# Optimization experiments

Measured on AMD Instinct MI355X. Metric: run time of the kernel, lower is better.

The kernel has to match this reference:

```python
import jax, jax.numpy as jnp
import numpy as np

TAU = 0.96      # init_tau
N_OUT = 48      # readout neurons (last n_out of the merged population)
V_TH = 1.0      # LIF firing threshold

@jax.custom_vjp
def spike_fn(v):
    # Heaviside firing with triangle surrogate gradient
    return (v >= V_TH).astype(v.dtype)

def _spike_fwd(v):
    return spike_fn(v), v

def _spike_bwd(v, g):
    # TriangleCall surrogate: grad = max(0, 1 - |v - v_th|)
    return (g * jnp.maximum(0.0, 1.0 - jnp.abs(v - V_TH)),)

spike_fn.defvjp(_spike_fwd, _spike_bwd)


def setup_inputs() -> dict:
    key = jax.random.key(0)
    k1, k2, k3, k4 = jax.random.split(key, 4)
    B, T, n_in = 256, 100, 512
    n_hidden, n_out = 2000, 48
    N = n_hidden + n_out  # 2048
    x = jax.random.uniform(k1, (B, T, n_in), dtype=jnp.float32)
    # nn.Linear default init U(-1/sqrt(fan_in), 1/sqrt(fan_in)), scaled by 3, frozen
    bound = 1.0 / np.sqrt(n_in)
    W_fc = 3.0 * jax.random.uniform(k2, (N, n_in), minval=-bound, maxval=bound, dtype=jnp.float32)
    recurrent = jax.random.uniform(k3, (N, N), dtype=jnp.float32) / np.sqrt(N)
    mask = jnp.ones((N, N), jnp.float32) - jnp.eye(N, dtype=jnp.float32)  # no self-connections
    binary = (jax.random.uniform(k4, (N, N)) > 0.3).astype(jnp.float32)
    return {"x": x, "W_fc": W_fc, "recurrent": recurrent, "mask": mask, "binary": binary}


def reference(x, W_fc, recurrent, mask, binary):
    B = x.shape[0]
    N = recurrent.shape[0]
    eff_rec = recurrent * mask * binary                    # [N, N]
    # feed-forward currents for all timesteps at once: [B, T, N]
    cur_in = jnp.einsum('btn,mn->btm', x, W_fc)

    def step(carry, c_t):
        mem, spike = carry                                 # each [B, N]
        cur = c_t + spike @ eff_rec                        # recurrent drive
        mem = TAU * mem * (1.0 - spike) + cur              # LIF decay + hard reset
        spike = spike_fn(mem)
        return (mem, spike), spike[:, -N_OUT:]

    init = (jnp.zeros((B, N), x.dtype), jnp.zeros((B, N), x.dtype))
    _, outs = jax.lax.scan(step, init, jnp.swapaxes(cur_in, 0, 1))  # [T, B, n_out]
    return jnp.swapaxes(outs, 0, 1)                        # [B, T, n_out]
```

## Files before the change

### kernel.cpp

```cpp
#include <hip/hip_runtime.h>

typedef unsigned short u16;
typedef signed char s8;
typedef __attribute__((ext_vector_type(8))) short short8;
typedef __attribute__((ext_vector_type(4))) float f32x4;
typedef __attribute__((ext_vector_type(4))) unsigned short u16x4;
typedef __attribute__((ext_vector_type(4))) int i32x4;
typedef __attribute__((ext_vector_type(4))) unsigned int u32x4;

#define TT 100
#define NB 256
#define NN 2048
#define KREC 4096
#define NPRE 2
#define EPS 0.25f
#define WMAXC 0.1325826f
#define INV_SW (127.0f / WMAXC)
#define S_DEQ (WMAXC / 16129.0f)

#define OFF_WH    0ull
#define OFF_WL    2097152ull
#define OFF_WQ    4194304ull
#define OFF_XH4   5242880ull
#define OFF_XL4   6291456ull
#define OFF_XQ    7340032ull
#define OFF_BC    20447232ull
#define OFF_COLS  37224448ull
#define OFF_PARTC 37232640ull
#define OFF_FFPRE 37494784ull
#define OFF_SPK   45883392ull
#define OFF_MEMB  46931968ull
#define OFF_PART  49029120ull
#define OFF_FLAGS 65806336ull
#define OFF_AF    65806400ull
#define OFF_SYNC  65806912ull

__device__ __forceinline__ u16 f2bf(float f){
    unsigned int x = __float_as_uint(f);
    x += 0x7fffu + ((x >> 16) & 1u);
    return (u16)(x >> 16);
}
__device__ __forceinline__ float bf2f(u16 u){
    return __uint_as_float(((unsigned int)u) << 16);
}

__global__ void prep_all(const float* __restrict__ x, const float* __restrict__ Wfc,
                         const float* __restrict__ rec, const float* __restrict__ msk,
                         const float* __restrict__ bin,
                         u16* __restrict__ Wh, u16* __restrict__ Wl, s8* __restrict__ Wq,
                         u16* __restrict__ xh4, u16* __restrict__ xl4, s8* __restrict__ xq,
                         u16* __restrict__ Bc, float* __restrict__ partc)
{
    __shared__ u16 hs[64][66];
    __shared__ u16 ls[64][66];
    __shared__ float redc[4][64];
    int bid = blockIdx.x;
    if (bid < 6400){
        int idx = bid * 256 + threadIdx.x;
        int b = idx / (TT * 64);
        int r = idx - b * (TT * 64);
        int t = r >> 6;
        int c = r & 63;
        const float* gx = x + ((size_t)b * TT + t) * 512 + (c << 3);
        f32x4 f0 = *reinterpret_cast<const f32x4*>(gx);
        f32x4 f1 = *reinterpret_cast<const f32x4*>(gx + 4);
        unsigned long long q = 0;
        #pragma unroll
        for (int i = 0; i < 4; ++i)
            q |= (unsigned long long)(unsigned)__float2int_rn(f0[i] * 127.0f) << (8 * i);
        #pragma unroll
        for (int i = 0; i < 4; ++i)
            q |= (unsigned long long)(unsigned)__float2int_rn(f1[i] * 127.0f) << (8 * (i + 4));
        size_t o = ((size_t)t * NB + b) * 512 + (c << 3);
        *reinterpret_cast<unsigned long long*>(xq + o) = q;
        if (t < 4){
            short8 vh, vl;
            #pragma unroll
            for (int i = 0; i < 4; ++i){
                u16 h0 = f2bf(f0[i]);
                vh[i] = (short)h0; vl[i] = (short)f2bf(f0[i] - bf2f(h0));
                u16 h1 = f2bf(f1[i]);
                vh[i + 4] = (short)h1; vl[i + 4] = (short)f2bf(f1[i] - bf2f(h1));
            }
            *reinterpret_cast<short8*>(xh4 + o) = vh;
            *reinterpret_cast<short8*>(xl4 + o) = vl;
        }
    } else if (bid < 10496){
        int idx = (bid - 6400) * 256 + threadIdx.x;
        float v = Wfc[idx];
        u16 h = f2bf(v);
        Wh[idx] = h;
        Wl[idx] = f2bf(v - bf2f(h));
        Wq[idx] = (s8)__float2int_rn(v * INV_SW);
    } else {
        int r2 = bid - 10496;
        int bx = r2 & 31, by = r2 >> 5;
        int tid = threadIdx.x;
        int tm = tid & 63, t4 = tid >> 6;
        int m0 = bx * 64, n0 = by * 64;
        float accl = 0.f;
        #pragma unroll
        for (int j = 0; j < 16; ++j){
            int nl = t4 + j * 4;
            size_t gi = (size_t)(n0 + nl) * NN + m0 + tm;
            float e = rec[gi] * msk[gi] * bin[gi];
            u16 h = f2bf(e);
            hs[nl][tm] = h;
            ls[nl][tm] = f2bf(e - bf2f(h));
            accl += e;
        }
        redc[t4][tm] = accl;
        __syncthreads();
        if (t4 == 0)
            partc[(size_t)by * NN + m0 + tm] =
                redc[0][tm] + redc[1][tm] + redc[2][tm] + redc[3][tm];
        #pragma unroll
        for (int j = 0; j < 16; ++j){
            int ml = t4 + j * 4;
            size_t o = (size_t)(m0 + ml) * KREC + n0 + tm;
            Bc[o]        = hs[tm][ml];
            Bc[o + 2048] = ls[tm][ml];
        }
    }
}

__global__ __launch_bounds__(512, 2) void fused_gemm(const s8* __restrict__ xq,
    const s8* __restrict__ Wq, const u16* __restrict__ xh4, const u16* __restrict__ xl4,
    const u16* __restrict__ Wh, const u16* __restrict__ Wl,
    const float* __restrict__ partc, float* __restrict__ cs, float* __restrict__ ffpre,
    int* __restrict__ AF, float* __restrict__ out)
{
    __shared__ u16 Ab[2][4096];
    __shared__ u16 Bb[2][8192];
    __shared__ float csL[256];
    __shared__ int redH[8];
    const int tid = threadIdx.x, lane = tid & 63, w = tid >> 6;
    const int l7 = lane & 7, l8 = lane >> 3;
    const int bid = blockIdx.x;

    if (bid >= 192){
        const int bid2 = bid - 192;
        const int logical = (bid2 & 7) * 200 + (bid2 >> 3);
        const int mt = logical >> 3;
        const int bn = logical & 7;
        const int wm = w >> 2, wn = w & 3;

        if (tid < 256){
            float s = 0.f;
            #pragma unroll
            for (int c = 0; c < 32; ++c) s += partc[(size_t)c * NN + bn * 256 + tid];
            csL[tid] = s;
        }

        char* As_ = reinterpret_cast<char*>(Ab);
        char* Bs_ = reinterpret_cast<char*>(Bb);
        const int row_s = tid >> 2, gr = tid & 3;
        const int swA = ((row_s << 6) | (gr << 4)) ^ ((row_s & 7) << 4);
        const s8* gA = xq + (size_t)(mt * 128 + row_s) * 512 + gr * 16;
        int swB[2];
        const s8* gBp[2];
        #pragma unroll
        for (int j = 0; j < 2; ++j){
            int rb = j * 128 + row_s;
            swB[j] = ((rb << 6) | (gr << 4)) ^ ((rb & 7) << 4);
            gBp[j] = Wq + (size_t)(bn * 256 + rb) * 512 + gr * 16;
        }

        *reinterpret_cast<u32x4*>(As_ + swA) = *reinterpret_cast<const u32x4*>(gA);
        #pragma unroll
        for (int j = 0; j < 2; ++j)
            *reinterpret_cast<u32x4*>(Bs_ + swB[j]) = *reinterpret_cast<const u32x4*>(gBp[j]);
        u32x4 na  = *reinterpret_cast<const u32x4*>(gA + 64);
        u32x4 nb0 = *reinterpret_cast<const u32x4*>(gBp[0] + 64);
        u32x4 nb1 = *reinterpret_cast<const u32x4*>(gBp[1] + 64);
        __syncthreads();

        i32x4 acc[4][4];
        #pragma unroll
        for (int mi = 0; mi < 4; ++mi)
            #pragma unroll
            for (int ni = 0; ni < 4; ++ni) acc[mi][ni] = (i32x4){0, 0, 0, 0};

        const int kgb = (lane >> 4) << 4;
        #pragma unroll
        for (int kt = 0; kt < 8; ++kt){
            const int sel = kt & 1;
            if (kt < 7){
                const int os = sel ^ 1;
                *reinterpret_cast<u32x4*>(As_ + os * 8192 + swA) = na;
                *reinterpret_cast<u32x4*>(Bs_ + os * 16384 + swB[0]) = nb0;
                *reinterpret_cast<u32x4*>(Bs_ + os * 16384 + swB[1]) = nb1;
                if (kt + 2 < 8){
                    na  = *reinterpret_cast<const u32x4*>(gA + (kt + 2) * 64);
                    nb0 = *reinterpret_cast<const u32x4*>(gBp[0] + (kt + 2) * 64);
                    nb1 = *reinterpret_cast<const u32x4*>(gBp[1] + (kt + 2) * 64);
                }
            }
            const char* ab = As_ + sel * 8192;
            const char* bb3 = Bs_ + sel * 16384;
            i32x4 afr[4];
            #pragma unroll
            for (int mi = 0; mi < 4; ++mi){
                int r = wm * 64 + mi * 16 + (lane & 15);
                int off = ((r << 6) | kgb) ^ ((r & 7) << 4);
                afr[mi] = *reinterpret_cast<const i32x4*>(ab + off);
            }
            #pragma unroll
            for (int ni = 0; ni < 4; ++ni){
                int r = wn * 64 + ni * 16 + (lane & 15);
                int off = ((r << 6) | kgb) ^ ((r & 7) << 4);
                i32x4 bfr = *reinterpret_cast<const i32x4*>(bb3 + off);
                #pragma unroll
                for (int mi = 0; mi < 4; ++mi)
                    acc[mi][ni] = __builtin_amdgcn_mfma_i32_16x16x64_i8(afr[mi], bfr, acc[mi][ni], 0, 0, 0);
            }
            __syncthreads();
        }

        const int r4 = (lane >> 4) << 2;
        const int cfrag = lane & 15;
        const int t_out = mt >> 1;
        int ok = 1;
        #pragma unroll
        for (int mi = 0; mi < 4; ++mi)
            #pragma unroll
            for (int ni = 0; ni < 4; ++ni){
                int nl = wn * 64 + ni * 16 + cfrag;
                int n = bn * 256 + nl;
                float csv = csL[nl];
                #pragma unroll
                for (int jj = 0; jj < 4; ++jj){
                    int m = mt * 128 + wm * 64 + mi * 16 + r4 + jj;
                    float v = (float)acc[mi][ni][jj] * S_DEQ + csv;
                    ok &= (v >= 1.0f + EPS) ? 1 : 0;
                    if (bn == 7 && n >= 2000){
                        int b = m & 255;
                        out[((size_t)b * TT + t_out) * 48 + (n - 2000)] = (v >= 1.0f) ? 1.f : 0.f;
                    }
                }
            }
        unsigned long long bb = __ballot(ok != 0);
        if (lane == 0) redH[w] = (bb == ~0ull) ? 1 : 0;
        __syncthreads();
        if (tid == 0){
            int a = 1;
            #pragma unroll
            for (int i = 0; i < 8; ++i) a &= redH[i];
            atomicAnd(&AF[t_out], a ? ~0 : 0);
        }
    } else {
        const int bn = bid & 15;
        const int mt = bid >> 4;
        const int wm = w >> 2, wn = w & 3;

        if (mt == 0 && tid < 128){
            float s = 0.f;
            #pragma unroll
            for (int c = 0; c < 32; ++c) s += partc[(size_t)c * NN + bn * 128 + tid];
            cs[bn * 128 + tid] = s;
        }

        auto load_tile = [&](int kt, short8* pa, short8* pb){
            int reg = kt >> 3;
            int kk = (kt & 7) * 64;
            const u16* ab = (reg == 2) ? xl4 : xh4;
            const u16* bb2 = (reg == 1) ? Wl : Wh;
            {
                int row = w * 8 + l8;
                pa[0] = *reinterpret_cast<const short8*>(ab + (size_t)(mt * 64 + row) * 512 + kk + (l7 << 3));
            }
            #pragma unroll
            for (int j = 0; j < 2; ++j){
                int chunk = w * 2 + j;
                int row = chunk * 8 + l8;
                pb[j] = *reinterpret_cast<const short8*>(bb2 + (size_t)(bn * 128 + row) * 512 + kk + (l7 << 3));
            }
        };
        auto write_tile = [&](int sel, const short8* pa, const short8* pb){
            *reinterpret_cast<short8*>(&Ab[sel][w * 512 + l8 * 64 + ((l7 ^ l8) << 3)]) = pa[0];
            #pragma unroll
            for (int j = 0; j < 2; ++j){
                int chunk = w * 2 + j;
                *reinterpret_cast<short8*>(&Bb[sel][chunk * 512 + l8 * 64 + ((l7 ^ l8) << 3)]) = pb[j];
            }
        };

        f32x4 zero = {0.f, 0.f, 0.f, 0.f};
        f32x4 acc[2][2];
        #pragma unroll
        for (int mi = 0; mi < 2; ++mi)
            #pragma unroll
            for (int ni = 0; ni < 2; ++ni) acc[mi][ni] = zero;

        short8 ra[1], rb[2], na[1], nb[2];
        load_tile(0, ra, rb);
        write_tile(0, ra, rb);
        __syncthreads();

        for (int kt = 0; kt < 24; ++kt){
            int sel = kt & 1;
            if (kt + 1 < 24) load_tile(kt + 1, na, nb);
            #pragma unroll
            for (int kk2 = 0; kk2 < 2; ++kk2){
                int ke = kk2 * 32 + ((lane >> 4) << 3);
                short8 af[2], bfr[2];
                #pragma unroll
                for (int mi = 0; mi < 2; ++mi){
                    int row = wm * 32 + mi * 16 + (lane & 15);
                    int byte = (row * 128 + ke * 2) ^ ((row & 7) << 4);
                    af[mi] = *reinterpret_cast<const short8*>(reinterpret_cast<const char*>(Ab[sel]) + byte);
                }
                #pragma unroll
                for (int ni = 0; ni < 2; ++ni){
                    int row = wn * 32 + ni * 16 + (lane & 15);
                    int byte = (row * 128 + ke * 2) ^ ((row & 7) << 4);
                    bfr[ni] = *reinterpret_cast<const short8*>(reinterpret_cast<const char*>(Bb[sel]) + byte);
                }
                #pragma unroll
                for (int mi = 0; mi < 2; ++mi)
                    #pragma unroll
                    for (int ni = 0; ni < 2; ++ni)
                        acc[mi][ni] = __builtin_amdgcn_mfma_f32_16x16x32_bf16(af[mi], bfr[ni], acc[mi][ni], 0, 0, 0);
            }
            if (kt + 1 < 24) write_tile((kt + 1) & 1, na, nb);
            __syncthreads();
        }

        const int r4 = (lane >> 4) << 2;
        const int c  = lane & 15;
        #pragma unroll
        for (int mi = 0; mi < 2; ++mi)
            #pragma unroll
            for (int ni = 0; ni < 2; ++ni){
                int n = bn * 128 + wn * 32 + ni * 16 + c;
                #pragma unroll
                for (int jj = 0; jj < 4; ++jj){
                    int m = mt * 64 + wm * 32 + mi * 16 + r4 + jj;
                    ffpre[(size_t)m * NN + n] = acc[mi][ni][jj];
                }
            }
    }
}


__device__ __forceinline__ void lif_finish(int b, int n0, const float mem[4], int t,
    u16* __restrict__ spk, float* __restrict__ memb, float* __restrict__ out,
    int* __restrict__ flags, int* red, int tid, int lane, int w)
{
    int s[4];
    u16x4 sv; f32x4 mv;
    #pragma unroll
    for (int k = 0; k < 4; ++k){
        s[k] = (mem[k] >= 1.0f) ? 1 : 0;
        sv[k] = s[k] ? (u16)0x3F80 : (u16)0;
        mv[k] = mem[k];
    }
    *reinterpret_cast<u16x4*>(spk + (size_t)b * NN + n0) = sv;
    *reinterpret_cast<f32x4*>(memb + (size_t)b * NN + n0) = mv;
    if (n0 >= 2000){
        #pragma unroll
        for (int k = 0; k < 4; ++k)
            out[((size_t)b * TT + t) * 48 + (n0 + k - 2000)] = s[k] ? 1.f : 0.f;
    }
    int af = s[0] & s[1] & s[2] & s[3];
    int az = !(s[0] | s[1] | s[2] | s[3]);
    unsigned long long ba = __ballot(af != 0);
    unsigned long long bz = __ballot(az != 0);
    if (lane == 0) red[w] = ((ba == ~0ull) ? 1 : 0) | ((bz == ~0ull) ? 2 : 0);
    __syncthreads();
    if (tid == 0){
        int a = 3;
        #pragma unroll
        for (int i = 0; i < 8; ++i) a &= red[i];
        atomicAnd(&flags[t], 0xFFFFFFFC | a);
    }
}

__global__ __launch_bounds__(512) void lif0(const float* __restrict__ ffpre,
    u16* __restrict__ spk, float* __restrict__ memb, float* __restrict__ out,
    int* __restrict__ flags)
{
    __shared__ int red[8];
    const int tid = threadIdx.x, lane = tid & 63, w = tid >> 6;
    const int b = blockIdx.x, n0 = tid << 2;
    f32x4 fe = *reinterpret_cast<const f32x4*>(ffpre + (size_t)b * NN + n0);
    float m[4];
    #pragma unroll
    for (int k = 0; k < 4; ++k) m[k] = fe[k];
    lif_finish(b, n0, m, 0, spk, memb, out, flags, red, tid, lane, w);
}

__global__ __launch_bounds__(512, 2) void gemm_pre(
    const u16* __restrict__ Bc, const u16* __restrict__ spk,
    const int* __restrict__ flags, float* __restrict__ part, int t)
{
    if (flags[t - 1] & 3) return;
    __shared__ u16 Ab[2][8192];
    __shared__ u16 Bb[2][8192];
    const int tid = threadIdx.x, lane = tid & 63, w = tid >> 6;
    const int l7 = lane & 7, l8 = lane >> 3;
    const int bid = blockIdx.x;
    const int bn = bid & 15, my = (bid >> 4) & 1, ks = bid >> 5;
    const int kstart = ks << 9, acol = kstart & 2047;
    const int wm = w >> 2, wn = w & 3;

    auto load_tile = [&](int kt, short8* pa, short8* pb){
        int k0 = kt * 64;
        #pragma unroll
        for (int j = 0; j < 2; ++j){
            int chunk = w * 2 + j;
            int row = chunk * 8 + l8;
            const u16* ga = spk + (size_t)(my * 128 + row) * NN + acol + k0 + (l7 << 3);
            pa[j] = *reinterpret_cast<const short8*>(ga);
            const u16* gb = Bc + (size_t)(bn * 128 + row) * KREC + kstart + k0 + (l7 << 3);
            pb[j] = *reinterpret_cast<const short8*>(gb);
        }
    };
    auto write_tile = [&](int sel, const short8* pa, const short8* pb){
        #pragma unroll
        for (int j = 0; j < 2; ++j){
            int chunk = w * 2 + j;
            int idx = chunk * 512 + l8 * 64 + ((l7 ^ l8) << 3);
            *reinterpret_cast<short8*>(&Ab[sel][idx]) = pa[j];
            *reinterpret_cast<short8*>(&Bb[sel][idx]) = pb[j];
        }
    };

    f32x4 zero = {0.f, 0.f, 0.f, 0.f};
    f32x4 acc[4][2];
    #pragma unroll
    for (int mi = 0; mi < 4; ++mi)
        #pragma unroll
        for (int ni = 0; ni < 2; ++ni) acc[mi][ni] = zero;

    short8 ra[2], rb[2], na[2], nb[2];
    load_tile(0, ra, rb);
    write_tile(0, ra, rb);
    __syncthreads();

    for (int kt = 0; kt < 8; ++kt){
        int sel = kt & 1;
        if (kt + 1 < 8) load_tile(kt + 1, na, nb);
        #pragma unroll
        for (int kk2 = 0; kk2 < 2; ++kk2){
            int ke = kk2 * 32 + ((lane >> 4) << 3);
            short8 af2[4], bfr[2];
            #pragma unroll
            for (int mi = 0; mi < 4; ++mi){
                int row = wm * 64 + mi * 16 + (lane & 15);
                int byte = (row * 128 + ke * 2) ^ ((row & 7) << 4);
                af2[mi] = *reinterpret_cast<const short8*>(reinterpret_cast<const char*>(Ab[sel]) + byte);
            }
            #pragma unroll
            for (int ni = 0; ni < 2; ++ni){
                int row = wn * 32 + ni * 16 + (lane & 15);
                int byte = (row * 128 + ke * 2) ^ ((row & 7) << 4);
                bfr[ni] = *reinterpret_cast<const short8*>(reinterpret_cast<const char*>(Bb[sel]) + byte);
            }
            #pragma unroll
            for (int mi = 0; mi < 4; ++mi)
                #pragma unroll
                for (int ni = 0; ni < 2; ++ni)
                    acc[mi][ni] = __builtin_amdgcn_mfma_f32_16x16x32_bf16(af2[mi], bfr[ni], acc[mi][ni], 0, 0, 0);
        }
        if (kt + 1 < 8) write_tile((kt + 1) & 1, na, nb);
        __syncthreads();
    }

    float* pp = part + (size_t)ks * (NB * NN);
    const int r4 = (lane >> 4) << 2;
    const int c  = lane & 15;
    #pragma unroll
    for (int mi = 0; mi < 4; ++mi)
        #pragma unroll
        for (int ni = 0; ni < 2; ++ni){
            int n = bn * 128 + wn * 32 + ni * 16 + c;
            #pragma unroll
            for (int jj = 0; jj < 4; ++jj){
                int b = my * 128 + wm * 64 + mi * 16 + r4 + jj;
                pp[(size_t)b * NN + n] = acc[mi][ni][jj];
            }
        }
}

__global__ __launch_bounds__(512) void lif_pre(const float* __restrict__ ffpre,
    const float* __restrict__ colsum, const float* __restrict__ part,
    const int* __restrict__ AF, u16* __restrict__ spk, float* __restrict__ memb,
    float* __restrict__ out, int* __restrict__ flags, int t)
{
    __shared__ int red[8];
    const int tid = threadIdx.x, lane = tid & 63, w = tid >> 6;
    const int b = blockIdx.x, n0 = tid << 2;
    int fl = flags[t - 1] & 3;
    float m[4];

    if (fl & 1){
        if (AF[t] != 0){
            if (b == 0 && tid == 0) flags[t] = 1;
            return;
        }
        f32x4 cs = *reinterpret_cast<const f32x4*>(colsum + n0);
        f32x4 fe = *reinterpret_cast<const f32x4*>(ffpre + ((size_t)t * NB + b) * NN + n0);
        #pragma unroll
        for (int k = 0; k < 4; ++k) m[k] = cs[k] + fe[k];
    } else if (fl & 2){
        f32x4 mb = *reinterpret_cast<const f32x4*>(memb + (size_t)b * NN + n0);
        f32x4 fe = *reinterpret_cast<const f32x4*>(ffpre + ((size_t)t * NB + b) * NN + n0);
        #pragma unroll
        for (int k = 0; k < 4; ++k) m[k] = 0.96f * mb[k] + fe[k];
    } else {
        f32x4 mb = *reinterpret_cast<const f32x4*>(memb + (size_t)b * NN + n0);
        u16x4 sp = *reinterpret_cast<const u16x4*>(spk + (size_t)b * NN + n0);
        f32x4 fe = *reinterpret_cast<const f32x4*>(ffpre + ((size_t)t * NB + b) * NN + n0);
        float p[4] = {0.f, 0.f, 0.f, 0.f};
        #pragma unroll
        for (int ks2 = 0; ks2 < 8; ++ks2){
            f32x4 pv = *reinterpret_cast<const f32x4*>(part + (size_t)ks2 * (NB * NN) + (size_t)b * NN + n0);
            #pragma unroll
            for (int k = 0; k < 4; ++k) p[k] += pv[k];
        }
        #pragma unroll
        for (int k = 0; k < 4; ++k){
            float sprev = sp[k] ? 1.f : 0.f;
            m[k] = 0.96f * mb[k] * (1.f - sprev) + p[k] + fe[k];
        }
    }
    lif_finish(b, n0, m, t, spk, memb, out, flags, red, tid, lane, w);
}

__global__ __launch_bounds__(512, 1) void snn_tail(
    const u16* __restrict__ Bc, const float* __restrict__ x, const float* __restrict__ Wfc,
    const float* __restrict__ colsum, const int* __restrict__ AF, const int* __restrict__ flags,
    u16* __restrict__ spk, float* __restrict__ memb, float* __restrict__ part,
    int* __restrict__ sync, float* __restrict__ out)
{
    __shared__ u16 Ab[2][8192];
    __shared__ u16 Bb[2][8192];
    __shared__ float xrow[512];
    __shared__ int red[8];
    __shared__ int bcast;
    __shared__ int firstbad;
    const int tid = threadIdx.x, lane = tid & 63, w = tid >> 6;
    const int l7 = lane & 7, l8 = lane >> 3;
    const int bid = blockIdx.x;
    int* cnt = sync;
    int* gen = sync + 1;
    int* vote = sync + 2;
    const int b_own = bid;
    const int n0 = tid << 2;
    const int bn = bid & 15, my = (bid >> 4) & 1, ks = bid >> 5;
    const int kstart = ks << 9, acol = kstart & 2047;
    const int wm = w >> 2, wn = w & 3;

    auto gbar = [&](){
        asm volatile("s_waitcnt vmcnt(0) lgkmcnt(0)" ::: "memory");
        __syncthreads();
        if (tid == 0){
            __threadfence();
            int g = __hip_atomic_load(gen, __ATOMIC_RELAXED, __HIP_MEMORY_SCOPE_AGENT);
            int a = __hip_atomic_fetch_add(cnt, 1, __ATOMIC_ACQ_REL, __HIP_MEMORY_SCOPE_AGENT);
            if (a == (int)gridDim.x - 1){
                __hip_atomic_store(cnt, 0, __ATOMIC_RELAXED, __HIP_MEMORY_SCOPE_AGENT);
                __hip_atomic_fetch_add(gen, 1, __ATOMIC_RELEASE, __HIP_MEMORY_SCOPE_AGENT);
            } else {
                while (__hip_atomic_load(gen, __ATOMIC_ACQUIRE, __HIP_MEMORY_SCOPE_AGENT) == g)
                    __builtin_amdgcn_s_sleep(2);
            }
            __threadfence();
        }
        __syncthreads();
    };

    auto wait_vote = [&](int t)->int{
        if (tid == 0){
            int v;
            while (((unsigned)(v = __hip_atomic_load(&vote[t], __ATOMIC_ACQUIRE, __HIP_MEMORY_SCOPE_AGENT)) >> 20) != 256u)
                __builtin_amdgcn_s_sleep(2);
            bcast = v;
        }
        __syncthreads();
        int v = bcast;
        __syncthreads();
        int naf = ((v & 0x3FF) == 256) ? 1 : 0;
        int naz = (((v >> 10) & 0x3FF) == 256) ? 2 : 0;
        return naf | naz;
    };

    auto finish_step = [&](f32x4 m, int t){
        int s[4];
        u16x4 sv;
        #pragma unroll
        for (int k = 0; k < 4; ++k){
            s[k] = (m[k] >= 1.0f) ? 1 : 0;
            sv[k] = s[k] ? (u16)0x3F80 : (u16)0;
        }
        *reinterpret_cast<u16x4*>(spk + (size_t)b_own * NN + n0) = sv;
        *reinterpret_cast<f32x4*>(memb + (size_t)b_own * NN + n0) = m;
        if (n0 >= 2000){
            #pragma unroll
            for (int k = 0; k < 4; ++k)
                out[((size_t)b_own * TT + t) * 48 + (n0 + k - 2000)] = s[k] ? 1.f : 0.f;
        }
        int af = s[0] & s[1] & s[2] & s[3];
        int az = !(s[0] | s[1] | s[2] | s[3]);
        unsigned long long ba = __ballot(af != 0);
        unsigned long long bz = __ballot(az != 0);
        if (lane == 0) red[w] = ((ba == ~0ull) ? 1 : 0) | ((bz == ~0ull) ? 2 : 0);
        __syncthreads();
        if (tid == 0){
            int a = 3;
            #pragma unroll
            for (int i = 0; i < 8; ++i) a &= red[i];
            __hip_atomic_fetch_add(&vote[t], (1 << 20) | (a & 1) | ((a >> 1) << 10),
                                   __ATOMIC_RELEASE, __HIP_MEMORY_SCOPE_AGENT);
        }
        __syncthreads();
    };

    auto load_ff = [&](int tq)->f32x4{
        __syncthreads();
        xrow[tid & 511] = x[((size_t)b_own * TT + tq) * 512 + (tid & 511)];
        __syncthreads();
        f32x4 f = {0.f, 0.f, 0.f, 0.f};
        for (int k = 0; k < 512; ++k){
            float xv = xrow[k];
            #pragma unroll
            for (int j = 0; j < 4; ++j)
                f[j] += xv * Wfc[(size_t)(n0 + j) * 512 + k];
        }
        return f;
    };

    int pv = flags[NPRE] & 3;
    int t = NPRE + 1;

    while (t < TT){
        if (pv & 1){
            if (tid == 0) firstbad = TT;
            __syncthreads();
            int idx = t + tid;
            if (idx < TT && AF[idx] == 0) atomicMin(&firstbad, idx);
            __syncthreads();
            int h = firstbad;
            if (h == TT) return;
            f32x4 cs = *reinterpret_cast<const f32x4*>(colsum + n0);
            f32x4 ffv = load_ff(h);
            f32x4 m;
            #pragma unroll
            for (int k = 0; k < 4; ++k) m[k] = cs[k] + ffv[k];
            finish_step(m, h);
            pv = wait_vote(h);
            t = h + 1;
        } else if (pv & 2){
            f32x4 ffv = load_ff(t);
            f32x4 mb = *reinterpret_cast<const f32x4*>(memb + (size_t)b_own * NN + n0);
            f32x4 m;
            #pragma unroll
            for (int k = 0; k < 4; ++k) m[k] = 0.96f * mb[k] + ffv[k];
            finish_step(m, t);
            pv = wait_vote(t);
            ++t;
        } else {
            gbar();
            auto load_tile = [&](int kt, short8* pa, short8* pb){
                int k0 = kt * 64;
                #pragma unroll
                for (int j = 0; j < 2; ++j){
                    int chunk = w * 2 + j;
                    int row = chunk * 8 + l8;
                    const u16* ga = spk + (size_t)(my * 128 + row) * NN + acol + k0 + (l7 << 3);
                    pa[j] = *reinterpret_cast<const short8*>(ga);
                    const u16* gb = Bc + (size_t)(bn * 128 + row) * KREC + kstart + k0 + (l7 << 3);
                    pb[j] = *reinterpret_cast<const short8*>(gb);
                }
            };
            auto write_tile = [&](int sel, const short8* pa, const short8* pb){
                #pragma unroll
                for (int j = 0; j < 2; ++j){
                    int chunk = w * 2 + j;
                    int idx = chunk * 512 + l8 * 64 + ((l7 ^ l8) << 3);
                    *reinterpret_cast<short8*>(&Ab[sel][idx]) = pa[j];
                    *reinterpret_cast<short8*>(&Bb[sel][idx]) = pb[j];
                }
            };

            f32x4 zero = {0.f, 0.f, 0.f, 0.f};
            f32x4 acc[4][2];
            #pragma unroll
            for (int mi = 0; mi < 4; ++mi)
                #pragma unroll
                for (int ni = 0; ni < 2; ++ni) acc[mi][ni] = zero;

            short8 ra[2], rb[2], na[2], nb[2];
            load_tile(0, ra, rb);
            write_tile(0, ra, rb);
            __syncthreads();

            for (int kt = 0; kt < 8; ++kt){
                int sel = kt & 1;
                if (kt + 1 < 8) load_tile(kt + 1, na, nb);
                #pragma unroll
                for (int kk2 = 0; kk2 < 2; ++kk2){
                    int ke = kk2 * 32 + ((lane >> 4) << 3);
                    short8 af2[4], bfr[2];
                    #pragma unroll
                    for (int mi = 0; mi < 4; ++mi){
                        int row = wm * 64 + mi * 16 + (lane & 15);
                        int byte = (row * 128 + ke * 2) ^ ((row & 7) << 4);
                        af2[mi] = *reinterpret_cast<const short8*>(reinterpret_cast<const char*>(Ab[sel]) + byte);
                    }
                    #pragma unroll
                    for (int ni = 0; ni < 2; ++ni){
                        int row = wn * 32 + ni * 16 + (lane & 15);
                        int byte = (row * 128 + ke * 2) ^ ((row & 7) << 4);
                        bfr[ni] = *reinterpret_cast<const short8*>(reinterpret_cast<const char*>(Bb[sel]) + byte);
                    }
                    #pragma unroll
                    for (int mi = 0; mi < 4; ++mi)
                        #pragma unroll
                        for (int ni = 0; ni < 2; ++ni)
                            acc[mi][ni] = __builtin_amdgcn_mfma_f32_16x16x32_bf16(af2[mi], bfr[ni], acc[mi][ni], 0, 0, 0);
                }
                if (kt + 1 < 8) write_tile((kt + 1) & 1, na, nb);
                __syncthreads();
            }

            float* pp = part + (size_t)ks * (NB * NN);
            const int r4 = (lane >> 4) << 2;
            const int c  = lane & 15;
            #pragma unroll
            for (int mi = 0; mi < 4; ++mi)
                #pragma unroll
                for (int ni = 0; ni < 2; ++ni){
                    int n = bn * 128 + wn * 32 + ni * 16 + c;
                    #pragma unroll
                    for (int jj = 0; jj < 4; ++jj){
                        int b = my * 128 + wm * 64 + mi * 16 + r4 + jj;
                        pp[(size_t)b * NN + n] = acc[mi][ni][jj];
                    }
                }
            gbar();

            f32x4 ffv = load_ff(t);
            f32x4 mb = *reinterpret_cast<const f32x4*>(memb + (size_t)b_own * NN + n0);
            u16x4 sp = *reinterpret_cast<const u16x4*>(spk + (size_t)b_own * NN + n0);
            float p[4] = {0.f, 0.f, 0.f, 0.f};
            #pragma unroll
            for (int ks2 = 0; ks2 < 8; ++ks2){
                f32x4 pvv = *reinterpret_cast<const f32x4*>(part + (size_t)ks2 * (NB * NN) + (size_t)b_own * NN + n0);
                #pragma unroll
                for (int k = 0; k < 4; ++k) p[k] += pvv[k];
            }
            f32x4 m;
            #pragma unroll
            for (int k = 0; k < 4; ++k){
                float sprev = sp[k] ? 1.f : 0.f;
                m[k] = 0.96f * mb[k] * (1.f - sprev) + p[k] + ffv[k];
            }
            finish_step(m, t);
            pv = wait_vote(t);
            ++t;
        }
    }
}

extern "C" void kernel_launch(void* const* d_in, const int* in_sizes, int n_in,
                              void* d_out, int out_size, void* d_ws, size_t ws_size,
                              hipStream_t stream)
{
    const float* x   = (const float*)d_in[0];
    const float* Wfc = (const float*)d_in[1];
    const float* rec = (const float*)d_in[2];
    const float* msk = (const float*)d_in[3];
    const float* bin = (const float*)d_in[4];
    float* out = (float*)d_out;
    char* ws = (char*)d_ws;

    u16* Wh      = (u16*)(ws + OFF_WH);
    u16* Wl      = (u16*)(ws + OFF_WL);
    s8*  Wq      = (s8*)(ws + OFF_WQ);
    u16* xh4     = (u16*)(ws + OFF_XH4);
    u16* xl4     = (u16*)(ws + OFF_XL4);
    s8*  xq      = (s8*)(ws + OFF_XQ);
    u16* Bc      = (u16*)(ws + OFF_BC);
    float* cs    = (float*)(ws + OFF_COLS);
    float* partc = (float*)(ws + OFF_PARTC);
    float* ffpre = (float*)(ws + OFF_FFPRE);
    u16* spk     = (u16*)(ws + OFF_SPK);
    float* memb  = (float*)(ws + OFF_MEMB);
    float* part  = (float*)(ws + OFF_PART);
    int* flags   = (int*)(ws + OFF_FLAGS);
    int* AF      = (int*)(ws + OFF_AF);
    int* sync    = (int*)(ws + OFF_SYNC);

    hipMemsetAsync(flags, 0xFF, 576, stream);
    hipMemsetAsync(sync, 0, 1024, stream);

    prep_all<<<11520, 256, 0, stream>>>(x, Wfc, rec, msk, bin, Wh, Wl, Wq, xh4, xl4, xq, Bc, partc);
    fused_gemm<<<1792, 512, 0, stream>>>(xq, Wq, xh4, xl4, Wh, Wl, partc, cs, ffpre, AF, out);
    lif0<<<256, 512, 0, stream>>>(ffpre, spk, memb, out, flags);
    for (int t = 1; t <= NPRE; ++t){
        gemm_pre<<<256, 512, 0, stream>>>(Bc, spk, flags, part, t);
        lif_pre<<<256, 512, 0, stream>>>(ffpre, cs, part, AF, spk, memb, out, flags, t);
    }
    snn_tail<<<256, 512, 0, stream>>>(Bc, x, Wfc, cs, AF, flags, spk, memb, part, sync, out);
}
```

Measured before the change: 129.0 us.

## Load int8 GEMM fragments directly from global memory, skipping LDS staging

The int8 feed-forward GEMM branch now has each lane load its MFMA A and B fragments straight from global memory instead of staging tiles through double-buffered swizzled LDS with per-iteration barriers. The per-k-step __syncthreads calls go away, leaving a single barrier after the loop, and the launch-bounds occupancy hint rises from 2 to 4 blocks per CU. In exchange, data shared across waves is now fetched redundantly from global memory or cache instead of being reused via LDS, and the higher occupancy hint may force register spills.

Result: slower. 190.7 us (+47.8%).

```diff
diff --git a/kernel.cpp b/kernel.cpp
--- a/kernel.cpp
+++ b/kernel.cpp
@@ -124,7 +124,7 @@
     }
 }
 
-__global__ __launch_bounds__(512, 2) void fused_gemm(const s8* __restrict__ xq,
+__global__ __launch_bounds__(512, 4) void fused_gemm(const s8* __restrict__ xq,
     const s8* __restrict__ Wq, const u16* __restrict__ xh4, const u16* __restrict__ xl4,
     const u16* __restrict__ Wh, const u16* __restrict__ Wl,
     const float* __restrict__ partc, float* __restrict__ cs, float* __restrict__ ffpre,
@@ -152,28 +152,10 @@
             csL[tid] = s;
         }
 
-        char* As_ = reinterpret_cast<char*>(Ab);
-        char* Bs_ = reinterpret_cast<char*>(Bb);
-        const int row_s = tid >> 2, gr = tid & 3;
-        const int swA = ((row_s << 6) | (gr << 4)) ^ ((row_s & 7) << 4);
-        const s8* gA = xq + (size_t)(mt * 128 + row_s) * 512 + gr * 16;
-        int swB[2];
-        const s8* gBp[2];
-        #pragma unroll
-        for (int j = 0; j < 2; ++j){
-            int rb = j * 128 + row_s;
-            swB[j] = ((rb << 6) | (gr << 4)) ^ ((rb & 7) << 4);
-            gBp[j] = Wq + (size_t)(bn * 256 + rb) * 512 + gr * 16;
-        }
-
-        *reinterpret_cast<u32x4*>(As_ + swA) = *reinterpret_cast<const u32x4*>(gA);
-        #pragma unroll
-        for (int j = 0; j < 2; ++j)
-            *reinterpret_cast<u32x4*>(Bs_ + swB[j]) = *reinterpret_cast<const u32x4*>(gBp[j]);
-        u32x4 na  = *reinterpret_cast<const u32x4*>(gA + 64);
-        u32x4 nb0 = *reinterpret_cast<const u32x4*>(gBp[0] + 64);
-        u32x4 nb1 = *reinterpret_cast<const u32x4*>(gBp[1] + 64);
-        __syncthreads();
+        const int lane15 = lane & 15;
+        const int lqb = (lane >> 4) << 4;
+        const s8* gAf = xq + (size_t)(mt * 128 + wm * 64 + lane15) * 512 + lqb;
+        const s8* gBf = Wq + (size_t)(bn * 256 + wn * 64 + lane15) * 512 + lqb;
 
         i32x4 acc[4][4];
         #pragma unroll
@@ -181,41 +163,22 @@
             #pragma unroll
             for (int ni = 0; ni < 4; ++ni) acc[mi][ni] = (i32x4){0, 0, 0, 0};
 
-        const int kgb = (lane >> 4) << 4;
-        #pragma unroll
+        #pragma unroll 2
         for (int kt = 0; kt < 8; ++kt){
-            const int sel = kt & 1;
-            if (kt < 7){
-                const int os = sel ^ 1;
-                *reinterpret_cast<u32x4*>(As_ + os * 8192 + swA) = na;
-                *reinterpret_cast<u32x4*>(Bs_ + os * 16384 + swB[0]) = nb0;
-                *reinterpret_cast<u32x4*>(Bs_ + os * 16384 + swB[1]) = nb1;
-                if (kt + 2 < 8){
-                    na  = *reinterpret_cast<const u32x4*>(gA + (kt + 2) * 64);
-                    nb0 = *reinterpret_cast<const u32x4*>(gBp[0] + (kt + 2) * 64);
-                    nb1 = *reinterpret_cast<const u32x4*>(gBp[1] + (kt + 2) * 64);
-                }
-            }
-            const char* ab = As_ + sel * 8192;
-            const char* bb3 = Bs_ + sel * 16384;
-            i32x4 afr[4];
-            #pragma unroll
-            for (int mi = 0; mi < 4; ++mi){
-                int r = wm * 64 + mi * 16 + (lane & 15);
-                int off = ((r << 6) | kgb) ^ ((r & 7) << 4);
-                afr[mi] = *reinterpret_cast<const i32x4*>(ab + off);
-            }
-            #pragma unroll
-            for (int ni = 0; ni < 4; ++ni){
-                int r = wn * 64 + ni * 16 + (lane & 15);
-                int off = ((r << 6) | kgb) ^ ((r & 7) << 4);
-                i32x4 bfr = *reinterpret_cast<const i32x4*>(bb3 + off);
+            i32x4 fa[4], fb[4];
+            #pragma unroll
+            for (int mi = 0; mi < 4; ++mi)
+                fa[mi] = *reinterpret_cast<const i32x4*>(gAf + mi * 8192 + kt * 64);
+            #pragma unroll
+            for (int ni = 0; ni < 4; ++ni)
+                fb[ni] = *reinterpret_cast<const i32x4*>(gBf + ni * 8192 + kt * 64);
+            #pragma unroll
+            for (int ni = 0; ni < 4; ++ni)
                 #pragma unroll
                 for (int mi = 0; mi < 4; ++mi)
-                    acc[mi][ni] = __builtin_amdgcn_mfma_i32_16x16x64_i8(afr[mi], bfr, acc[mi][ni], 0, 0, 0);
-            }
-            __syncthreads();
-        }
+                    acc[mi][ni] = __builtin_amdgcn_mfma_i32_16x16x64_i8(fa[mi], fb[ni], acc[mi][ni], 0, 0, 0);
+        }
+        __syncthreads();
 
         const int r4 = (lane >> 4) << 2;
         const int cfrag = lane & 15;
```
